# Kernel optimization log

Measured on AMD Instinct MI355X. Metric: run time of the kernel, lower is better.

Reference implementation:

```python
import jax, jax.numpy as jnp
import numpy as np

DT = 1e-3   # time step [s] (geometry.dt)
H = 10.0    # grid spacing [m] (geometry.h)

# Staggered-grid first differences (2nd-order accurate on the staggered grid).
# Periodic wrap at the boundary via roll; the damping layer d absorbs there.

def _dplus(f, ax):
    return (jnp.roll(f, -1, axis=ax) - f) / H

def _dminus(f, ax):
    return (f - jnp.roll(f, 1, axis=ax)) / H


def setup_inputs() -> dict:
    key = jax.random.key(0)
    ks = jax.random.split(key, 9)
    B, NZ, NX = 4, 2048, 2048
    vp = 1500.0 + 2500.0 * jax.random.uniform(ks[0], (NZ, NX), jnp.float32)   # P velocity [m/s]
    vs = vp / 1.73                                                            # S velocity (Poisson solid)
    rho = 1000.0 + 1000.0 * jax.random.uniform(ks[1], (NZ, NX), jnp.float32)  # density [kg/m^3]
    fields = {}
    for i, name in enumerate(['vx', 'vz', 'txx', 'tzz', 'txz']):
        fields[name] = 1e-3 * jax.random.normal(ks[2 + i], (B, NZ, NX), jnp.float32)
    d = 50.0 * jax.random.uniform(ks[8], (NZ, NX), jnp.float32)               # PML damping profile
    return dict(vp=vp, vs=vs, rho=rho, **fields, d=d)


def reference(vp, vs, rho, vx, vz, txx, tzz, txz, d):
    # Lame parameters from (vp, vs, rho)
    mu = rho * vs * vs
    lam = rho * vp * vp - 2.0 * mu
    # Split-free damping update: y = (1-c)/(1+c) * y_old + dt/(1+c) * rhs
    c = 0.5 * DT * d            # [nz, nx], broadcasts over shot dim
    a = (1.0 - c) / (1.0 + c)
    b = DT / (1.0 + c)
    # --- velocity update (leapfrog: uses old stresses) ---
    vx_new = a * vx + b * (_dminus(txx, -1) + _dminus(txz, -2)) / rho
    vz_new = a * vz + b * (_dplus(txz, -1) + _dplus(tzz, -2)) / rho
    # --- stress update (uses new velocities) ---
    vx_x = _dplus(vx_new, -1)
    vz_z = _dminus(vz_new, -2)
    txx_new = a * txx + b * ((lam + 2.0 * mu) * vx_x + lam * vz_z)
    tzz_new = a * tzz + b * ((lam + 2.0 * mu) * vz_z + lam * vx_x)
    txz_new = a * txz + b * mu * (_dplus(vx_new, -2) + _dminus(vz_new, -1))
    # hidden state for next time step: [5, B, nz, nx]
    return jnp.stack([vx_new, vz_new, txx_new, tzz_new, txz_new])
```

## Files before the change

### kernel.cpp

```cpp
#include <hip/hip_runtime.h>


constexpr int NZ = 2048;
constexpr int NX = 2048;
constexpr int B  = 4;
constexpr int PLANE = NZ * NX;
constexpr int VOL   = B * PLANE;
constexpr float DT    = 1e-3f;
constexpr float INV_H = 0.1f;
constexpr int NBLK  = (PLANE / 4) / 256;
constexpr int NXCD  = 8;
constexpr int BLK_PER_XCD = NBLK / NXCD;

typedef float f32x4 __attribute__((ext_vector_type(4)));

__device__ __forceinline__ float rcpf(float x) { return __builtin_amdgcn_rcpf(x); }
__device__ __forceinline__ float4 ld4(const float* __restrict__ p) {
    return *reinterpret_cast<const float4*>(p);
}
__device__ __forceinline__ void st4(float* __restrict__ p,
                                    float a, float b, float c, float d) {
    f32x4 v = {a, b, c, d};
    *reinterpret_cast<f32x4*>(p) = v;
}

__global__ __launch_bounds__(256) void wave_fused_v9(
    const float* __restrict__ vp,  const float* __restrict__ vs,
    const float* __restrict__ rho,
    const float* __restrict__ vx,  const float* __restrict__ vz,
    const float* __restrict__ txx, const float* __restrict__ tzz,
    const float* __restrict__ txz,
    const float* __restrict__ dd,
    float* __restrict__ out)
{
    const int bid = blockIdx.x;
    const int sb  = (bid & (NXCD - 1)) * BLK_PER_XCD + (bid >> 3);
    const int t   = sb * blockDim.x + threadIdx.x;
    const int xg = (t & (NX / 4 - 1)) << 2;
    const int z  = t >> 9;
    const int zp = (z + 1) & (NZ - 1);
    const int zm = (z - 1) & (NZ - 1);
    const int xm1 = (xg - 1) & (NX - 1);
    const int xp4 = (xg + 4) & (NX - 1);
    const int rz  = z  * NX;
    const int rzp = zp * NX;
    const int rzm = zm * NX;

    float dz6[6], rz6[6];
    {
        const float4 d4 = ld4(dd + rz + xg);
        dz6[0] = dd[rz + xm1]; dz6[1] = d4.x; dz6[2] = d4.y;
        dz6[3] = d4.z;         dz6[4] = d4.w; dz6[5] = dd[rz + xp4];
        const float4 r4 = ld4(rho + rz + xg);
        rz6[0] = rho[rz + xm1]; rz6[1] = r4.x; rz6[2] = r4.y;
        rz6[3] = r4.z;          rz6[4] = r4.w; rz6[5] = rho[rz + xp4];
    }
    float avz[6], bvz[6], inv_c[4];
    #pragma unroll
    for (int j = 0; j < 6; ++j) {
        const float c   = 0.5f * DT * dz6[j];
        const float inv = rcpf(1.0f + c);
        avz[j] = (1.0f - c) * inv;
        bvz[j] = DT * INV_H * inv * rcpf(rz6[j]);
        if (j >= 1 && j <= 4) inv_c[j - 1] = inv;
    }
    float avzp[4], bvzp[4], avzm[4], bvzm[4];
    {
        const float4 dp = ld4(dd + rzp + xg), dm = ld4(dd + rzm + xg);
        const float4 rp = ld4(rho + rzp + xg), rm = ld4(rho + rzm + xg);
        const float dpa[4] = {dp.x, dp.y, dp.z, dp.w};
        const float dma[4] = {dm.x, dm.y, dm.z, dm.w};
        const float rpa[4] = {rp.x, rp.y, rp.z, rp.w};
        const float rma[4] = {rm.x, rm.y, rm.z, rm.w};
        #pragma unroll
        for (int k = 0; k < 4; ++k) {
            float c = 0.5f * DT * dpa[k];
            float inv = rcpf(1.0f + c);
            avzp[k] = (1.0f - c) * inv;
            bvzp[k] = DT * INV_H * inv * rcpf(rpa[k]);
            c = 0.5f * DT * dma[k];
            inv = rcpf(1.0f + c);
            avzm[k] = (1.0f - c) * inv;
            bvzm[k] = DT * INV_H * inv * rcpf(rma[k]);
        }
    }
    float q1[4], q2[4], q3[4];
    {
        const float4 vp4 = ld4(vp + rz + xg), vs4 = ld4(vs + rz + xg);
        const float vpa[4] = {vp4.x, vp4.y, vp4.z, vp4.w};
        const float vsa[4] = {vs4.x, vs4.y, vs4.z, vs4.w};
        #pragma unroll
        for (int k = 0; k < 4; ++k) {
            const float r   = rz6[k + 1];
            const float muv = r * vsa[k] * vsa[k];
            const float lam = r * vpa[k] * vpa[k] - 2.0f * muv;
            const float bsH = DT * INV_H * inv_c[k];
            q1[k] = bsH * (lam + 2.0f * muv);
            q2[k] = bsH * lam;
            q3[k] = bsH * muv;
        }
    }

    #pragma unroll 1
    for (int b = 0; b < B; ++b) {
        const int b3  = b * PLANE;
        const int cz  = b3 + rz  + xg;
        const int czp = b3 + rzp + xg;
        const int czm = b3 + rzm + xg;

        float txxz[6], txzz[6], tzzz[5], tzzzp[5], txxzp[5];
        float txzzm[5];
        float vxz[5];
        float vzz[5];
        {
            float4 m;
            m = ld4(txx + cz);
            txxz[1] = m.x; txxz[2] = m.y; txxz[3] = m.z; txxz[4] = m.w;
            txxz[0] = txx[b3 + rz + xm1];  txxz[5] = txx[b3 + rz + xp4];
            m = ld4(txz + cz);
            txzz[1] = m.x; txzz[2] = m.y; txzz[3] = m.z; txzz[4] = m.w;
            txzz[0] = txz[b3 + rz + xm1];  txzz[5] = txz[b3 + rz + xp4];
            m = ld4(tzz + cz);
            tzzz[1] = m.x; tzzz[2] = m.y; tzzz[3] = m.z; tzzz[4] = m.w;
            tzzz[0] = tzz[b3 + rz + xm1];
            m = ld4(tzz + czp);
            tzzzp[1] = m.x; tzzzp[2] = m.y; tzzzp[3] = m.z; tzzzp[4] = m.w;
            tzzzp[0] = tzz[b3 + rzp + xm1];
            m = ld4(txx + czp);
            txxzp[1] = m.x; txxzp[2] = m.y; txxzp[3] = m.z; txxzp[4] = m.w;
            txxzp[0] = txx[b3 + rzp + xm1];
            m = ld4(txz + czm);
            txzzm[0] = m.x; txzzm[1] = m.y; txzzm[2] = m.z; txzzm[3] = m.w;
            txzzm[4] = txz[b3 + rzm + xp4];
            m = ld4(vx + cz);
            vxz[0] = m.x; vxz[1] = m.y; vxz[2] = m.z; vxz[3] = m.w;
            vxz[4] = vx[b3 + rz + xp4];
            m = ld4(vz + cz);
            vzz[1] = m.x; vzz[2] = m.y; vzz[3] = m.z; vzz[4] = m.w;
            vzz[0] = vz[b3 + rz + xm1];
        }
        const float4 tp4 = ld4(txz + czp);
        const float4 tm4 = ld4(tzz + czm);
        const float4 vxp4 = ld4(vx + czp);
        const float4 vzm4 = ld4(vz + czm);
        const float txzzp[4] = {tp4.x, tp4.y, tp4.z, tp4.w};
        const float tzzzm[4] = {tm4.x, tm4.y, tm4.z, tm4.w};
        const float vxzp[4]  = {vxp4.x, vxp4.y, vxp4.z, vxp4.w};
        const float vzzm[4]  = {vzm4.x, vzm4.y, vzm4.z, vzm4.w};

        float vxn_z[5];
        #pragma unroll
        for (int k = 0; k < 5; ++k)
            vxn_z[k] = avz[k + 1] * vxz[k]
                     + bvz[k + 1] * ((txxz[k + 1] - txxz[k])
                                   + (txzz[k + 1] - txzzm[k]));
        float vzn_z[5];
        #pragma unroll
        for (int k = 0; k < 5; ++k)
            vzn_z[k] = avz[k] * vzz[k]
                     + bvz[k] * ((txzz[k + 1] - txzz[k])
                               + (tzzzp[k] - tzzz[k]));
        float vxn_zp[4];
        #pragma unroll
        for (int k = 0; k < 4; ++k)
            vxn_zp[k] = avzp[k] * vxzp[k]
                      + bvzp[k] * ((txxzp[k + 1] - txxzp[k])
                                 + (txzzp[k] - txzz[k + 1]));
        float vzn_zm[4];
        #pragma unroll
        for (int k = 0; k < 4; ++k)
            vzn_zm[k] = avzm[k] * vzzm[k]
                      + bvzm[k] * ((txzzm[k + 1] - txzzm[k])
                                 + (tzzz[k + 1] - tzzzm[k]));

        float oxx[4], ozz[4], oxz[4];
        #pragma unroll
        for (int k = 0; k < 4; ++k) {
            const float dvx = vxn_z[k + 1] - vxn_z[k];
            const float dvz = vzn_z[k + 1] - vzn_zm[k];
            oxx[k] = avz[k + 1] * txxz[k + 1] + q1[k] * dvx + q2[k] * dvz;
            ozz[k] = avz[k + 1] * tzzz[k + 1] + q1[k] * dvz + q2[k] * dvx;
            oxz[k] = avz[k + 1] * txzz[k + 1]
                   + q3[k] * ((vxn_zp[k] - vxn_z[k])
                            + (vzn_z[k + 1] - vzn_z[k]));
        }

        st4(out + 0 * VOL + cz, vxn_z[0], vxn_z[1], vxn_z[2], vxn_z[3]);
        st4(out + 1 * VOL + cz, vzn_z[1], vzn_z[2], vzn_z[3], vzn_z[4]);
        st4(out + 2 * VOL + cz, oxx[0], oxx[1], oxx[2], oxx[3]);
        st4(out + 3 * VOL + cz, ozz[0], ozz[1], ozz[2], ozz[3]);
        st4(out + 4 * VOL + cz, oxz[0], oxz[1], oxz[2], oxz[3]);
    }
}

extern "C" void kernel_launch(void* const* d_in, const int* in_sizes, int n_in,
                              void* d_out, int out_size, void* d_ws, size_t ws_size,
                              hipStream_t stream) {
    const float* vp  = (const float*)d_in[0];
    const float* vs  = (const float*)d_in[1];
    const float* rho = (const float*)d_in[2];
    const float* vx  = (const float*)d_in[3];
    const float* vz  = (const float*)d_in[4];
    const float* txx = (const float*)d_in[5];
    const float* tzz = (const float*)d_in[6];
    const float* txz = (const float*)d_in[7];
    const float* dd  = (const float*)d_in[8];
    float* out = (float*)d_out;

    const int threads = 256;
    const int blocks  = NBLK;
    hipLaunchKernelGGL(wave_fused_v9, dim3(blocks), dim3(threads), 0, stream,
                       vp, vs, rho, vx, vz, txx, tzz, txz, dd, out);
}
```

Measured before the change: 609.2 us.

## Stage 2D field tiles with halos in LDS instead of redundant global loads

Blocks now cover a 16x64 2D tile rather than a half row. For each shot the five wavefield inputs are cooperatively loaded into shared memory, including one halo row above and below and 16-column halos, and all stencil neighbours are then read from LDS. This removes the repeated global and L2 loads of neighbouring rows and the unaligned scalar halo loads. The cost is extra barriers per shot, about 36KB of LDS per block that may limit occupancy, and halo over-fetch of roughly 1.7x per tile.

```diff
diff --git a/kernel.cpp b/kernel.cpp
--- a/kernel.cpp
+++ b/kernel.cpp
@@ -8,8 +8,13 @@
 constexpr int VOL   = B * PLANE;
 constexpr float DT    = 1e-3f;
 constexpr float INV_H = 0.1f;
-constexpr int NBLK  = (PLANE / 4) / 256;
-constexpr int NXCD  = 8;
+
+constexpr int ZB = 16;
+constexpr int XR = 64;
+constexpr int NROW = ZB + 2;
+constexpr int RST  = 100;
+constexpr int NBLK = PLANE / (ZB * XR);
+constexpr int NXCD = 8;
 constexpr int BLK_PER_XCD = NBLK / NXCD;
 
 typedef float f32x4 __attribute__((ext_vector_type(4)));
@@ -24,7 +29,7 @@
     *reinterpret_cast<f32x4*>(p) = v;
 }
 
-__global__ __launch_bounds__(256) void wave_fused_v9(
+__global__ __launch_bounds__(256) void wave_fused_v10(
     const float* __restrict__ vp,  const float* __restrict__ vs,
     const float* __restrict__ rho,
     const float* __restrict__ vx,  const float* __restrict__ vz,
@@ -33,25 +38,34 @@
     const float* __restrict__ dd,
     float* __restrict__ out)
 {
+    __shared__ float lds[5 * NROW * RST];
+
     const int bid = blockIdx.x;
     const int sb  = (bid & (NXCD - 1)) * BLK_PER_XCD + (bid >> 3);
-    const int t   = sb * blockDim.x + threadIdx.x;
-    const int xg = (t & (NX / 4 - 1)) << 2;
-    const int z  = t >> 9;
-    const int zp = (z + 1) & (NZ - 1);
-    const int zm = (z - 1) & (NZ - 1);
-    const int xm1 = (xg - 1) & (NX - 1);
-    const int xp4 = (xg + 4) & (NX - 1);
+    const int tz  = sb >> 5;
+    const int tx  = sb & 31;
+    const int z0  = tz << 4;
+    const int x0  = tx << 6;
+    const int tid = threadIdx.x;
+    const int xt  = tid & 15;
+    const int zt  = tid >> 4;
+
+    const int z   = z0 + zt;
+    const int x   = x0 + (xt << 2);
+    const int zp  = (z + 1) & (NZ - 1);
+    const int zm  = (z - 1) & (NZ - 1);
+    const int xm1 = (x - 1) & (NX - 1);
+    const int xp4 = (x + 4) & (NX - 1);
     const int rz  = z  * NX;
     const int rzp = zp * NX;
     const int rzm = zm * NX;
 
     float dz6[6], rz6[6];
     {
-        const float4 d4 = ld4(dd + rz + xg);
+        const float4 d4 = ld4(dd + rz + x);
         dz6[0] = dd[rz + xm1]; dz6[1] = d4.x; dz6[2] = d4.y;
         dz6[3] = d4.z;         dz6[4] = d4.w; dz6[5] = dd[rz + xp4];
-        const float4 r4 = ld4(rho + rz + xg);
+        const float4 r4 = ld4(rho + rz + x);
         rz6[0] = rho[rz + xm1]; rz6[1] = r4.x; rz6[2] = r4.y;
         rz6[3] = r4.z;          rz6[4] = r4.w; rz6[5] = rho[rz + xp4];
     }
@@ -66,8 +80,8 @@
     }
     float avzp[4], bvzp[4], avzm[4], bvzm[4];
     {
-        const float4 dp = ld4(dd + rzp + xg), dm = ld4(dd + rzm + xg);
-        const float4 rp = ld4(rho + rzp + xg), rm = ld4(rho + rzm + xg);
+        const float4 dp = ld4(dd + rzp + x), dm = ld4(dd + rzm + x);
+        const float4 rp = ld4(rho + rzp + x), rm = ld4(rho + rzm + x);
         const float dpa[4] = {dp.x, dp.y, dp.z, dp.w};
         const float dma[4] = {dm.x, dm.y, dm.z, dm.w};
         const float rpa[4] = {rp.x, rp.y, rp.z, rp.w};
@@ -86,7 +100,7 @@
     }
     float q1[4], q2[4], q3[4];
     {
-        const float4 vp4 = ld4(vp + rz + xg), vs4 = ld4(vs + rz + xg);
+        const float4 vp4 = ld4(vp + rz + x), vs4 = ld4(vs + rz + x);
         const float vpa[4] = {vp4.x, vp4.y, vp4.z, vp4.w};
         const float vsa[4] = {vs4.x, vs4.y, vs4.z, vs4.w};
         #pragma unroll
@@ -101,52 +115,90 @@
         }
     }
 
+    const int lx = 16 + (xt << 2);
+    const int rT = (0 * NROW + zt) * RST;
+    const int rX = (1 * NROW + zt) * RST;
+    const int rZ = (2 * NROW + zt) * RST;
+    const int rV = (3 * NROW + zt) * RST;
+    const int rW = (4 * NROW + zt) * RST;
+
     #pragma unroll 1
     for (int b = 0; b < B; ++b) {
-        const int b3  = b * PLANE;
-        const int cz  = b3 + rz  + xg;
-        const int czp = b3 + rzp + xg;
-        const int czm = b3 + rzm + xg;
-
+        const int b3 = b * PLANE;
+
+        if (b) __syncthreads();
+
+        {
+            const float* const ap0 = txx + b3;
+            const float* const ap1 = txz + b3;
+            const float* const ap2 = tzz + b3;
+            const float* const ap3 = vx  + b3;
+            const float* const ap4 = vz  + b3;
+            #pragma unroll
+            for (int a = 0; a < 5; ++a) {
+                const float* const ap = (a == 0) ? ap0 : (a == 1) ? ap1
+                                      : (a == 2) ? ap2 : (a == 3) ? ap3 : ap4;
+                #pragma unroll
+                for (int k = 0; k < 2; ++k) {
+                    const int idx = k * 256 + tid;
+                    if (idx < NROW * 24) {
+                        const int r  = idx / 24;
+                        const int c  = idx % 24;
+                        const int gz = (z0 - 1 + r) & (NZ - 1);
+                        const int gx = (x0 - 16 + (c << 2)) & (NX - 1);
+                        const f32x4 v =
+                            *reinterpret_cast<const f32x4*>(ap + gz * NX + gx);
+                        *reinterpret_cast<f32x4*>(
+                            &lds[(a * NROW + r) * RST + (c << 2)]) = v;
+                    }
+                }
+            }
+        }
+        __syncthreads();
+
+        auto L4 = [&](int off) -> f32x4 {
+            return *reinterpret_cast<const f32x4*>(&lds[off]);
+        };
         float txxz[6], txzz[6], tzzz[5], tzzzp[5], txxzp[5];
-        float txzzm[5];
-        float vxz[5];
-        float vzz[5];
+        float txzzm[5], vxz[5], vzz[5];
+        float txzzp[4], tzzzm[4], vxzp[4], vzzm[4];
         {
-            float4 m;
-            m = ld4(txx + cz);
+            f32x4 m;
+            m = L4(rT + RST + lx);
             txxz[1] = m.x; txxz[2] = m.y; txxz[3] = m.z; txxz[4] = m.w;
-            txxz[0] = txx[b3 + rz + xm1];  txxz[5] = txx[b3 + rz + xp4];
-            m = ld4(txz + cz);
+            txxz[0] = lds[rT + RST + lx - 1];
+            txxz[5] = lds[rT + RST + lx + 4];
+            m = L4(rX + RST + lx);
             txzz[1] = m.x; txzz[2] = m.y; txzz[3] = m.z; txzz[4] = m.w;
-            txzz[0] = txz[b3 + rz + xm1];  txzz[5] = txz[b3 + rz + xp4];
-            m = ld4(tzz + cz);
+            txzz[0] = lds[rX + RST + lx - 1];
+            txzz[5] = lds[rX + RST + lx + 4];
+            m = L4(rZ + RST + lx);
             tzzz[1] = m.x; tzzz[2] = m.y; tzzz[3] = m.z; tzzz[4] = m.w;
-            tzzz[0] = tzz[b3 + rz + xm1];
-            m = ld4(tzz + czp);
+            tzzz[0] = lds[rZ + RST + lx - 1];
+            m = L4(rZ + 2 * RST + lx);
             tzzzp[1] = m.x; tzzzp[2] = m.y; tzzzp[3] = m.z; tzzzp[4] = m.w;
-            tzzzp[0] = tzz[b3 + rzp + xm1];
-            m = ld4(txx + czp);
+            tzzzp[0] = lds[rZ + 2 * RST + lx - 1];
+            m = L4(rT + 2 * RST + lx);
             txxzp[1] = m.x; txxzp[2] = m.y; txxzp[3] = m.z; txxzp[4] = m.w;
-            txxzp[0] = txx[b3 + rzp + xm1];
-            m = ld4(txz + czm);
+            txxzp[0] = lds[rT + 2 * RST + lx - 1];
+            m = L4(rX + lx);
             txzzm[0] = m.x; txzzm[1] = m.y; txzzm[2] = m.z; txzzm[3] = m.w;
-            txzzm[4] = txz[b3 + rzm + xp4];
-            m = ld4(vx + cz);
+            txzzm[4] = lds[rX + lx + 4];
+            m = L4(rV + RST + lx);
             vxz[0] = m.x; vxz[1] = m.y; vxz[2] = m.z; vxz[3] = m.w;
-            vxz[4] = vx[b3 + rz + xp4];
-            m = ld4(vz + cz);
+            vxz[4] = lds[rV + RST + lx + 4];
+            m = L4(rW + RST + lx);
             vzz[1] = m.x; vzz[2] = m.y; vzz[3] = m.z; vzz[4] = m.w;
-            vzz[0] = vz[b3 + rz + xm1];
-        }
-        const float4 tp4 = ld4(txz + czp);
-        const float4 tm4 = ld4(tzz + czm);
-        const float4 vxp4 = ld4(vx + czp);
-        const float4 vzm4 = ld4(vz + czm);
-        const float txzzp[4] = {tp4.x, tp4.y, tp4.z, tp4.w};
-        const float tzzzm[4] = {tm4.x, tm4.y, tm4.z, tm4.w};
-        const float vxzp[4]  = {vxp4.x, vxp4.y, vxp4.z, vxp4.w};
-        const float vzzm[4]  = {vzm4.x, vzm4.y, vzm4.z, vzm4.w};
+            vzz[0] = lds[rW + RST + lx - 1];
+            m = L4(rX + 2 * RST + lx);
+            txzzp[0] = m.x; txzzp[1] = m.y; txzzp[2] = m.z; txzzp[3] = m.w;
+            m = L4(rZ + lx);
+            tzzzm[0] = m.x; tzzzm[1] = m.y; tzzzm[2] = m.z; tzzzm[3] = m.w;
+            m = L4(rV + 2 * RST + lx);
+            vxzp[0] = m.x; vxzp[1] = m.y; vxzp[2] = m.z; vxzp[3] = m.w;
+            m = L4(rW + lx);
+            vzzm[0] = m.x; vzzm[1] = m.y; vzzm[2] = m.z; vzzm[3] = m.w;
+        }
 
         float vxn_z[5];
         #pragma unroll
@@ -185,6 +237,7 @@
                             + (vzn_z[k + 1] - vzn_z[k]));
         }
 
+        const int cz = b3 + rz + x;
         st4(out + 0 * VOL + cz, vxn_z[0], vxn_z[1], vxn_z[2], vxn_z[3]);
         st4(out + 1 * VOL + cz, vzn_z[1], vzn_z[2], vzn_z[3], vzn_z[4]);
         st4(out + 2 * VOL + cz, oxx[0], oxx[1], oxx[2], oxx[3]);
@@ -209,6 +262,6 @@
 
     const int threads = 256;
     const int blocks  = NBLK;
-    hipLaunchKernelGGL(wave_fused_v9, dim3(blocks), dim3(threads), 0, stream,
+    hipLaunchKernelGGL(wave_fused_v10, dim3(blocks), dim3(threads), 0, stream,
                        vp, vs, rho, vx, vz, txx, tzz, txz, dd, out);
 }
```

Result: slower. 647.7 us (+6.3%).
